# Performance work log

Measured on AMD Instinct MI355X. Metric: run time of the kernel, lower is better.

## Reference

```python
import jax, jax.numpy as jnp
import numpy as np

N, E, B, L, D, H = 50000, 800000, 64, 32, 256, 256


def setup_inputs() -> dict:
    key = jax.random.key(0)
    ks = jax.random.split(key, 20)
    s = 0.05
    inp = {
        'x': jax.random.normal(ks[0], (N, D), jnp.float32),
        'edge_index': jax.random.randint(ks[1], (2, E), 0, N),
        'batch': jnp.sort(jax.random.randint(ks[2], (N,), 0, B)),
        'paths': jax.random.randint(ks[3], (B, L), 0, N),
        # SAGEConv1: lin_l (aggregated neighbors, with bias) + lin_r (root, no bias)
        'w1l': jax.random.normal(ks[4], (D, H), jnp.float32) * s,
        'b1l': jnp.zeros((H,), jnp.float32),
        'w1r': jax.random.normal(ks[5], (D, H), jnp.float32) * s,
        # SAGEConv2
        'w2l': jax.random.normal(ks[6], (H, H), jnp.float32) * s,
        'b2l': jnp.zeros((H,), jnp.float32),
        'w2r': jax.random.normal(ks[7], (H, H), jnp.float32) * s,
        # LSTM (gate order i,f,g,o as in torch)
        'w_ih': jax.random.normal(ks[8], (4 * H, H), jnp.float32) * s,
        'w_hh': jax.random.normal(ks[9], (4 * H, H), jnp.float32) * s,
        'b_ih': jnp.zeros((4 * H,), jnp.float32),
        'b_hh': jnp.zeros((4 * H,), jnp.float32),
        # scorer MLP
        'wm1': jax.random.normal(ks[10], (2 * H, H), jnp.float32) * s,
        'bm1': jnp.zeros((H,), jnp.float32),
        'wm2': jax.random.normal(ks[11], (H, 1), jnp.float32) * s,
        'bm2': jnp.zeros((1,), jnp.float32),
    }
    return inp


def sage_conv(x, src, dst, wl, bl, wr):
    # mean-aggregate neighbor features (messages flow src -> dst)
    agg = jax.ops.segment_sum(x[src], dst, num_segments=N)
    deg = jax.ops.segment_sum(jnp.ones((src.shape[0],), x.dtype), dst, num_segments=N)
    mean = agg / jnp.maximum(deg, 1.0)[:, None]
    return mean @ wl + bl + x @ wr


def lstm_last_hidden(seq, w_ih, w_hh, b_ih, b_hh):
    # seq: [B, L, H] -> hn: [B, H]
    h0 = jnp.zeros((seq.shape[0], H), seq.dtype)
    c0 = jnp.zeros_like(h0)

    def step(carry, xt):
        h, c = carry
        gates = xt @ w_ih.T + b_ih + h @ w_hh.T + b_hh
        i, f, g, o = jnp.split(gates, 4, axis=-1)
        c = jax.nn.sigmoid(f) * c + jax.nn.sigmoid(i) * jnp.tanh(g)
        h = jax.nn.sigmoid(o) * jnp.tanh(c)
        return (h, c), None

    (hn, _), _ = jax.lax.scan(step, (h0, c0), jnp.swapaxes(seq, 0, 1))
    return hn


def reference(x, edge_index, batch, paths, w1l, b1l, w1r, w2l, b2l, w2r,
              w_ih, w_hh, b_ih, b_hh, wm1, bm1, wm2, bm2):
    src, dst = edge_index[0], edge_index[1]
    h = jax.nn.relu(sage_conv(x, src, dst, w1l, b1l, w1r))
    node_emb = sage_conv(h, src, dst, w2l, b2l, w2r)  # [N, H]

    # global mean pool per graph
    gsum = jax.ops.segment_sum(node_emb, batch, num_segments=B)
    gcnt = jax.ops.segment_sum(jnp.ones((N,), node_emb.dtype), batch, num_segments=B)
    graph_emb = gsum / jnp.maximum(gcnt, 1.0)[:, None]  # [B, H]

    path_seq = node_emb[paths]  # [B, L, H]
    path_emb = lstm_last_hidden(path_seq, w_ih, w_hh, b_ih, b_hh)  # [B, H]

    combined = jnp.concatenate([graph_emb, path_emb], axis=-1)  # [B, 2H]
    scores = jax.nn.relu(combined @ wm1 + bm1) @ wm2 + bm2  # [B, 1]
    return scores.reshape(-1)  # torch.cat of per-path [1] scores -> [B]
```

## Files before the change

kernel.cpp:

```cpp
#include <hip/hip_runtime.h>

namespace {

constexpr int NN = 50000;
constexpr int NE = 800000;
constexpr int NB = 64;
constexpr int NL = 32;
constexpr int ND = 256;
constexpr int NSCAN = 196;

typedef __attribute__((ext_vector_type(8))) short short8v;
typedef __attribute__((ext_vector_type(4))) float float4v;

__device__ __forceinline__ float sigf(float x){ return 1.0f/(1.0f + __expf(-x)); }

__device__ __forceinline__ ushort rne_bf16(float f){
  uint u = __float_as_uint(f);
  return (ushort)((u + 0x7FFFu + ((u >> 16) & 1u)) >> 16);
}
__device__ __forceinline__ float bf2f(ushort u){ return __uint_as_float((uint)u << 16); }

__device__ __forceinline__ void split8(float4 fa, float4 fb, uint4& h, uint4& lo){
  uint a0=__float_as_uint(fa.x), a1=__float_as_uint(fa.y), a2=__float_as_uint(fa.z), a3=__float_as_uint(fa.w);
  uint b0=__float_as_uint(fb.x), b1=__float_as_uint(fb.y), b2=__float_as_uint(fb.z), b3=__float_as_uint(fb.w);
  h.x = (a0>>16) | (a1 & 0xFFFF0000u);
  h.y = (a2>>16) | (a3 & 0xFFFF0000u);
  h.z = (b0>>16) | (b1 & 0xFFFF0000u);
  h.w = (b2>>16) | (b3 & 0xFFFF0000u);
  float r0 = fa.x - __uint_as_float(a0 & 0xFFFF0000u);
  float r1 = fa.y - __uint_as_float(a1 & 0xFFFF0000u);
  float r2 = fa.z - __uint_as_float(a2 & 0xFFFF0000u);
  float r3 = fa.w - __uint_as_float(a3 & 0xFFFF0000u);
  float r4 = fb.x - __uint_as_float(b0 & 0xFFFF0000u);
  float r5 = fb.y - __uint_as_float(b1 & 0xFFFF0000u);
  float r6 = fb.z - __uint_as_float(b2 & 0xFFFF0000u);
  float r7 = fb.w - __uint_as_float(b3 & 0xFFFF0000u);
  lo.x = (__float_as_uint(r0)>>16) | (__float_as_uint(r1) & 0xFFFF0000u);
  lo.y = (__float_as_uint(r2)>>16) | (__float_as_uint(r3) & 0xFFFF0000u);
  lo.z = (__float_as_uint(r4)>>16) | (__float_as_uint(r5) & 0xFFFF0000u);
  lo.w = (__float_as_uint(r6)>>16) | (__float_as_uint(r7) & 0xFFFF0000u);
}

__global__ void k_hist(const int* __restrict__ dst, int* __restrict__ cnt){
  int stride = gridDim.x * blockDim.x;
  for (int e = blockIdx.x*blockDim.x + threadIdx.x; e < NE; e += stride)
    atomicAdd(&cnt[dst[e]], 1);
}

__global__ void k_scan_block(const int* __restrict__ cnt, int* __restrict__ offs,
                             int* __restrict__ bsum){
  __shared__ int s[256];
  const int t = threadIdx.x, i = blockIdx.x*256 + t;
  int v = cnt[i];
  s[t] = v; __syncthreads();
  #pragma unroll
  for (int off = 1; off < 256; off <<= 1){
    int x = (t >= off) ? s[t-off] : 0;
    __syncthreads();
    s[t] += x;
    __syncthreads();
  }
  offs[i] = s[t] - v;
  if (t == 255) bsum[blockIdx.x] = s[255];
}

__global__ void k_scan_top(const int* __restrict__ bsum, int* __restrict__ bsum2){
  __shared__ int s[256];
  const int t = threadIdx.x;
  int v = (t < NSCAN) ? bsum[t] : 0;
  s[t] = v; __syncthreads();
  #pragma unroll
  for (int off = 1; off < 256; off <<= 1){
    int x = (t >= off) ? s[t-off] : 0;
    __syncthreads();
    s[t] += x;
    __syncthreads();
  }
  if (t < NSCAN) bsum2[t] = s[t] - v;
}

__global__ void k_scan_add(int* __restrict__ offs, const int* __restrict__ bsum2,
                           int* __restrict__ cursor){
  const int i = blockIdx.x*256 + threadIdx.x;
  int v = offs[i] + bsum2[blockIdx.x];
  offs[i] = v;
  cursor[i] = v;
}

__global__ void k_fill(const int* __restrict__ src, const int* __restrict__ dst,
                       int* __restrict__ cursor, int* __restrict__ csr){
  int stride = gridDim.x * blockDim.x;
  for (int e = blockIdx.x*blockDim.x + threadIdx.x; e < NE; e += stride){
    int d = dst[e];
    int pos = atomicAdd(&cursor[d], 1);
    csr[pos] = src[e];
  }
}

__global__ void k_tobf16(const float* __restrict__ in, ushort* __restrict__ out){
  const int i = blockIdx.x*blockDim.x + threadIdx.x;
  const float4 a = ((const float4*)in)[i*2];
  const float4 b = ((const float4*)in)[i*2+1];
  ushort o[8] = { rne_bf16(a.x), rne_bf16(a.y), rne_bf16(a.z), rne_bf16(a.w),
                  rne_bf16(b.x), rne_bf16(b.y), rne_bf16(b.z), rne_bf16(b.w) };
  ((uint4*)out)[i] = *(uint4*)o;
}

__launch_bounds__(256, 8)
__global__ void k_gather_bf16(const ushort* __restrict__ feat, const int* __restrict__ offs,
                              const int* __restrict__ csr, float* __restrict__ out){
  __shared__ float4 sp[256];
  const int u = blockIdx.x, t = threadIdx.x;
  const int w = t >> 6, l = t & 63;
  const int beg = offs[u], end = offs[u+1];
  const int lc = l * 4;
  float a0 = 0.f, a1 = 0.f, a2 = 0.f, a3 = 0.f;
  int e = beg + w;
  for (; e + 4 < end; e += 8){
    int s0 = csr[e], s1 = csr[e+4];
    ushort4 v0 = *(const ushort4*)(feat + (long long)s0*ND + lc);
    ushort4 v1 = *(const ushort4*)(feat + (long long)s1*ND + lc);
    a0 += bf2f(v0.x) + bf2f(v1.x);
    a1 += bf2f(v0.y) + bf2f(v1.y);
    a2 += bf2f(v0.z) + bf2f(v1.z);
    a3 += bf2f(v0.w) + bf2f(v1.w);
  }
  if (e < end){
    int s0 = csr[e];
    ushort4 v0 = *(const ushort4*)(feat + (long long)s0*ND + lc);
    a0 += bf2f(v0.x); a1 += bf2f(v0.y); a2 += bf2f(v0.z); a3 += bf2f(v0.w);
  }
  sp[t] = make_float4(a0, a1, a2, a3);
  __syncthreads();
  if (t < 64){
    float4 p0 = sp[t], p1 = sp[64+t], p2 = sp[128+t], p3 = sp[192+t];
    float inv = 1.0f / fmaxf((float)(end - beg), 1.0f);
    float4 r;
    r.x = (p0.x + p1.x + p2.x + p3.x) * inv;
    r.y = (p0.y + p1.y + p2.y + p3.y) * inv;
    r.z = (p0.z + p1.z + p2.z + p3.z) * inv;
    r.w = (p0.w + p1.w + p2.w + p3.w) * inv;
    *(float4*)(out + (long long)u*ND + t*4) = r;
  }
}

__global__ void k_wsplit(const float* __restrict__ wl, const float* __restrict__ wr,
                         ushort* __restrict__ WtH, ushort* __restrict__ WtL){
  const int k = blockIdx.x;
  const int n = threadIdx.x;
  float v = (k < 256) ? wl[k*256 + n] : wr[(k-256)*256 + n];
  uint u = __float_as_uint(v);
  float r = v - __uint_as_float(u & 0xFFFF0000u);
  const int wc = n >> 6, nt = (n >> 4) & 3, lm = n & 15;
  const int kk = k >> 5, lq = (k >> 3) & 3, j = k & 7;
  const long long idx = (long long)(((wc*4 + nt)*16 + kk)*64 + lq*16 + lm)*8 + j;
  WtH[idx] = (ushort)(u >> 16);
  WtL[idx] = (ushort)(__float_as_uint(r) >> 16);
}

__launch_bounds__(256, 2)
__global__ void k_gemm_mfma(const float* __restrict__ A1, const float* __restrict__ A2,
                            const ushort* __restrict__ WtH, const ushort* __restrict__ WtL,
                            const float* __restrict__ bias, float* __restrict__ C,
                            ushort* __restrict__ Cb, int relu)
{
  __shared__ float eb[16*260];
  const int t  = threadIdx.x;
  const int w  = t >> 6;
  const int l  = t & 63;
  const int lm = l & 15;
  const int lq = l >> 4;
  const int m0 = blockIdx.x * 64;

  const uint4* BH4 = (const uint4*)WtH;
  const uint4* BL4 = (const uint4*)WtL;

  const float4v vzero = {0.f, 0.f, 0.f, 0.f};
  float4v acc[4][4];
  #pragma unroll
  for (int i = 0; i < 4; ++i)
    #pragma unroll
    for (int j = 0; j < 4; ++j) acc[i][j] = vzero;

  long long arow[4];
  #pragma unroll
  for (int mt = 0; mt < 4; ++mt){
    int row = m0 + mt*16 + lm;
    row = (row < NN) ? row : (NN - 1);
    arow[mt] = (long long)row * ND;
  }
  int bbase[4];
  #pragma unroll
  for (int nt = 0; nt < 4; ++nt) bbase[nt] = (w*4 + nt)*1024 + l;

  auto ldB = [&](int kk, uint4* bh, uint4* bl){
    #pragma unroll
    for (int nt = 0; nt < 4; ++nt){
      int idx = bbase[nt] + kk*64;
      bh[nt] = BH4[idx];
      bl[nt] = BL4[idx];
    }
  };
  auto ldA = [&](int kk, uint4* ah, uint4* al){
    const float* Ab = (kk < 8) ? A1 : A2;
    const int koff = (kk & 7)*32 + lq*8;
    #pragma unroll
    for (int mt = 0; mt < 4; ++mt){
      const float* p = Ab + arow[mt] + koff;
      float4 fa = *(const float4*)p;
      float4 fb = *(const float4*)(p + 4);
      split8(fa, fb, ah[mt], al[mt]);
    }
  };

  uint4 bhb[2][4], blb[2][4], ahb[2][4], alb[2][4];
  ldB(0, bhb[0], blb[0]);
  ldA(0, ahb[0], alb[0]);

  #pragma unroll
  for (int kk = 0; kk < 16; ++kk){
    const int cur = kk & 1, nx = cur ^ 1;
    if (kk < 15){
      ldB(kk + 1, bhb[nx], blb[nx]);
      ldA(kk + 1, ahb[nx], alb[nx]);
    }
    #pragma unroll
    for (int nt = 0; nt < 4; ++nt){
      short8v bh = *(short8v*)&bhb[cur][nt];
      short8v bl = *(short8v*)&blb[cur][nt];
      #pragma unroll
      for (int mt = 0; mt < 4; ++mt){
        short8v ah = *(short8v*)&ahb[cur][mt];
        short8v al = *(short8v*)&alb[cur][mt];
        acc[mt][nt] = __builtin_amdgcn_mfma_f32_16x16x32_bf16(ah, bh, acc[mt][nt], 0, 0, 0);
        acc[mt][nt] = __builtin_amdgcn_mfma_f32_16x16x32_bf16(al, bh, acc[mt][nt], 0, 0, 0);
        acc[mt][nt] = __builtin_amdgcn_mfma_f32_16x16x32_bf16(ah, bl, acc[mt][nt], 0, 0, 0);
      }
    }
  }

  float bvv[4];
  #pragma unroll
  for (int nt = 0; nt < 4; ++nt) bvv[nt] = bias[w*64 + nt*16 + lm];

  #pragma unroll
  for (int mt = 0; mt < 4; ++mt){
    #pragma unroll
    for (int nt = 0; nt < 4; ++nt){
      #pragma unroll
      for (int r = 0; r < 4; ++r){
        float v = acc[mt][nt][r] + bvv[nt];
        if (relu) v = fmaxf(v, 0.f);
        eb[(lq*4 + r)*260 + w*64 + nt*16 + lm] = v;
      }
    }
    __syncthreads();
    #pragma unroll
    for (int i = 0; i < 4; ++i){
      int idx = i*256 + t;
      int rr  = idx >> 6;
      int c4  = (idx & 63) * 4;
      int grow = m0 + mt*16 + rr;
      if (grow < NN){
        float4 fv = *(float4*)&eb[rr*260 + c4];
        *(float4*)(C + (long long)grow*ND + c4) = fv;
        if (Cb){
          ushort ub[4] = { rne_bf16(fv.x), rne_bf16(fv.y), rne_bf16(fv.z), rne_bf16(fv.w) };
          *(ushort4*)(Cb + (long long)grow*ND + c4) = *(ushort4*)ub;
        }
      }
    }
    __syncthreads();
  }
}

__launch_bounds__(256, 3)
__global__ void k_xgate(const float* __restrict__ emb, const int* __restrict__ paths,
                        const float* __restrict__ w_ih, const float* __restrict__ b_ih,
                        const float* __restrict__ b_hh, float* __restrict__ xg)
{
  __shared__ float As[16][68];
  __shared__ float Ws[16][260];
  const int t  = threadIdx.x;
  const int m0 = blockIdx.x * 64;
  const int g0 = blockIdx.y * 256;
  const int rg = t >> 5, cg = t & 31;
  const int sm = t >> 2, sj = (t & 3) * 4;

  float acc[8][8];
  #pragma unroll
  for (int i = 0; i < 8; ++i)
    #pragma unroll
    for (int j = 0; j < 8; ++j) acc[i][j] = 0.f;

  const int node = paths[m0 + sm];
  const float* arow = emb  + (long long)node*ND;
  const float* wrow = w_ih + (long long)(g0 + t)*ND;

  for (int k0 = 0; k0 < 256; k0 += 16){
    float4 av = *(const float4*)(arow + k0 + sj);
    float4 q0 = *(const float4*)(wrow + k0 + 0);
    float4 q1 = *(const float4*)(wrow + k0 + 4);
    float4 q2 = *(const float4*)(wrow + k0 + 8);
    float4 q3 = *(const float4*)(wrow + k0 + 12);
    __syncthreads();
    As[sj+0][sm]=av.x; As[sj+1][sm]=av.y; As[sj+2][sm]=av.z; As[sj+3][sm]=av.w;
    Ws[ 0][t]=q0.x; Ws[ 1][t]=q0.y; Ws[ 2][t]=q0.z; Ws[ 3][t]=q0.w;
    Ws[ 4][t]=q1.x; Ws[ 5][t]=q1.y; Ws[ 6][t]=q1.z; Ws[ 7][t]=q1.w;
    Ws[ 8][t]=q2.x; Ws[ 9][t]=q2.y; Ws[10][t]=q2.z; Ws[11][t]=q2.w;
    Ws[12][t]=q3.x; Ws[13][t]=q3.y; Ws[14][t]=q3.z; Ws[15][t]=q3.w;
    __syncthreads();
    #pragma unroll
    for (int k = 0; k < 16; ++k){
      float a[8], b[8];
      *(float4*)&a[0] = *(const float4*)&As[k][rg*8];
      *(float4*)&a[4] = *(const float4*)&As[k][rg*8+4];
      *(float4*)&b[0] = *(const float4*)&Ws[k][cg*8];
      *(float4*)&b[4] = *(const float4*)&Ws[k][cg*8+4];
      #pragma unroll
      for (int i = 0; i < 8; ++i)
        #pragma unroll
        for (int j = 0; j < 8; ++j)
          acc[i][j] = fmaf(a[i], b[j], acc[i][j]);
    }
  }

  float bv[8];
  #pragma unroll
  for (int j = 0; j < 8; ++j){ int g = g0 + cg*8 + j; bv[j] = b_ih[g] + b_hh[g]; }
  #pragma unroll
  for (int i = 0; i < 8; ++i){
    int row = m0 + rg*8 + i;
    float o[8];
    #pragma unroll
    for (int j = 0; j < 8; ++j) o[j] = acc[i][j] + bv[j];
    *(float4*)(xg + (long long)row*1024 + g0 + cg*8 + 0) = *(float4*)&o[0];
    *(float4*)(xg + (long long)row*1024 + g0 + cg*8 + 4) = *(float4*)&o[4];
  }
}

__launch_bounds__(256, 4)
__global__ void k_lstm_step(const float* __restrict__ h_in, float* __restrict__ h_out,
                            float* __restrict__ c_state, const float* __restrict__ xg,
                            const float* __restrict__ w_hh, int tstep)
{
  __shared__ float ws[4*256];
  __shared__ float hs[32*260];
  __shared__ float part[2*128];
  __shared__ float gs[128];
  const int t  = threadIdx.x;
  const int u  = blockIdx.x >> 1;
  const int b0 = (blockIdx.x & 1) * 32;

  {
    int gate = t >> 6, c4 = (t & 63) * 4;
    float4 v = *(const float4*)(w_hh + (long long)(gate*256 + u)*256 + c4);
    *(float4*)&ws[gate*256 + c4] = v;
  }
  #pragma unroll
  for (int i = 0; i < 8; ++i){
    int idx = i*256 + t;
    int b = idx >> 6, c4 = (idx & 63) * 4;
    float4 v = *(const float4*)(h_in + (long long)(b0 + b)*256 + c4);
    *(float4*)&hs[b*260 + c4] = v;
  }
  __syncthreads();

  const int b  = t & 31;
  const int g  = (t >> 5) & 3;
  const int kd = t >> 7;
  float s = 0.f;
  const float* hp = &hs[b*260 + kd*128];
  const float* wp = &ws[g*256 + kd*128];
  #pragma unroll
  for (int k4 = 0; k4 < 32; ++k4){
    float4 h4 = *(const float4*)(hp + k4*4);
    float4 w4 = *(const float4*)(wp + k4*4);
    s += h4.x*w4.x + h4.y*w4.y + h4.z*w4.z + h4.w*w4.w;
  }
  part[kd*128 + b*4 + g] = s;
  __syncthreads();

  if (t < 128){
    int bb = t >> 2, gg = t & 3;
    const float* xp = xg + ((long long)(b0 + bb)*NL + tstep)*1024;
    gs[t] = part[t] + part[128 + t] + xp[gg*256 + u];
  }
  __syncthreads();

  if (t < 32){
    float gi = gs[t*4+0], gf = gs[t*4+1], gG = gs[t*4+2], go = gs[t*4+3];
    int bb = b0 + t;
    float c_old = c_state[bb*256 + u];
    float c_new = sigf(gf)*c_old + sigf(gi)*tanhf(gG);
    c_state[bb*256 + u] = c_new;
    h_out[bb*256 + u] = sigf(go)*tanhf(c_new);
  }
}

__global__ void k_pool(const float* __restrict__ emb, const int* __restrict__ batch,
                       float* __restrict__ gsum, float* __restrict__ gcnt)
{
  __shared__ int bs[256];
  const int t  = threadIdx.x;
  const int n0 = blockIdx.x * 256;
  {
    int n = n0 + t;
    bs[t] = (n < NN) ? batch[n] : -1;
  }
  __syncthreads();
  int cur = bs[0];
  float acc = 0.f; int cnt = 0;
  for (int j = 0; j < 256; ++j){
    int nn = n0 + j;
    if (nn >= NN) break;
    int g = bs[j];
    if (g != cur){
      unsafeAtomicAdd(&gsum[cur*256 + t], acc);
      if (t == 0) unsafeAtomicAdd(&gcnt[cur], (float)cnt);
      acc = 0.f; cnt = 0; cur = g;
    }
    acc += emb[(long long)nn*256 + t];
    ++cnt;
  }
  if (cnt > 0 && cur >= 0){
    unsafeAtomicAdd(&gsum[cur*256 + t], acc);
    if (t == 0) unsafeAtomicAdd(&gcnt[cur], (float)cnt);
  }
}

__global__ void k_score(const float* __restrict__ gsum, const float* __restrict__ gcnt,
                        const float* __restrict__ hfin, const float* __restrict__ wm1,
                        const float* __restrict__ bm1, const float* __restrict__ wm2,
                        const float* __restrict__ bm2, float* __restrict__ out)
{
  __shared__ float cs[512];
  __shared__ float red[4];
  const int b = blockIdx.x, t = threadIdx.x;
  float inv = 1.0f / fmaxf(gcnt[b], 1.0f);
  cs[t]       = gsum[b*256 + t] * inv;
  cs[256 + t] = hfin[b*256 + t];
  __syncthreads();
  float v = 0.f;
  #pragma unroll 4
  for (int k = 0; k < 512; ++k) v = fmaf(cs[k], wm1[(long long)k*256 + t], v);
  v = fmaxf(v + bm1[t], 0.f) * wm2[t];
  #pragma unroll
  for (int off = 32; off > 0; off >>= 1) v += __shfl_down(v, off, 64);
  if ((t & 63) == 0) red[t >> 6] = v;
  __syncthreads();
  if (t == 0) out[b] = red[0] + red[1] + red[2] + red[3] + bm2[0];
}

}

extern "C" void kernel_launch(void* const* d_in, const int* in_sizes, int n_in,
                              void* d_out, int out_size, void* d_ws, size_t ws_size,
                              hipStream_t stream)
{
  const float* x     = (const float*)d_in[0];
  const int*   eidx  = (const int*)  d_in[1];
  const int*   batch = (const int*)  d_in[2];
  const int*   paths = (const int*)  d_in[3];
  const float* w1l   = (const float*)d_in[4];
  const float* b1l   = (const float*)d_in[5];
  const float* w1r   = (const float*)d_in[6];
  const float* w2l   = (const float*)d_in[7];
  const float* b2l   = (const float*)d_in[8];
  const float* w2r   = (const float*)d_in[9];
  const float* w_ih  = (const float*)d_in[10];
  const float* w_hh  = (const float*)d_in[11];
  const float* b_ih  = (const float*)d_in[12];
  const float* b_hh  = (const float*)d_in[13];
  const float* wm1   = (const float*)d_in[14];
  const float* bm1   = (const float*)d_in[15];
  const float* wm2   = (const float*)d_in[16];
  const float* bm2   = (const float*)d_in[17];

  const int* src = eidx;
  const int* dst = eidx + NE;

  float* w    = (float*)d_ws;
  float* bufA = w;
  float* bufB = bufA + (long long)NN*ND;
  float* xg   = bufB + (long long)NN*ND;
  float* gsum = xg   + 2048*1024;
  float* gcnt = gsum + NB*ND;
  float* h0   = gcnt + 64;
  float* c0   = h0   + NB*ND;
  float* h1   = c0   + NB*ND;
  ushort* wt1H = (ushort*)(h1 + NB*ND);
  ushort* wt1L = wt1H + 256*512;
  ushort* wt2H = wt1L + 256*512;
  ushort* wt2L = wt2H + 256*512;
  ushort* fb16 = wt2L + 256*512;

  int* cnt    = (int*)xg;
  int* offs   = cnt    + 50432;
  int* cursor = offs   + 50432;
  int* bsum   = cursor + 50432;
  int* bsum2  = bsum   + 256;
  int* csr    = bsum2  + 256;

  k_wsplit<<<512, 256, 0, stream>>>(w1l, w1r, wt1H, wt1L);
  k_wsplit<<<512, 256, 0, stream>>>(w2l, w2r, wt2H, wt2L);

  k_tobf16<<<(NN*ND/8 + 255)/256, 256, 0, stream>>>(x, fb16);

  hipMemsetAsync(cnt, 0, 50432*sizeof(int), stream);
  k_hist<<<1024, 256, 0, stream>>>(dst, cnt);
  k_scan_block<<<NSCAN, 256, 0, stream>>>(cnt, offs, bsum);
  k_scan_top<<<1, 256, 0, stream>>>(bsum, bsum2);
  k_scan_add<<<NSCAN, 256, 0, stream>>>(offs, bsum2, cursor);
  k_fill<<<1024, 256, 0, stream>>>(src, dst, cursor, csr);

  k_gather_bf16<<<NN, 256, 0, stream>>>(fb16, offs, csr, bufA);
  k_gemm_mfma<<<(NN+63)/64, 256, 0, stream>>>(bufA, x, wt1H, wt1L, b1l, bufB, fb16, 1);

  k_gather_bf16<<<NN, 256, 0, stream>>>(fb16, offs, csr, bufA);
  k_gemm_mfma<<<(NN+63)/64, 256, 0, stream>>>(bufA, bufB, wt2H, wt2L, b2l, bufA, (ushort*)nullptr, 0);

  hipMemsetAsync(gsum, 0, (NB*ND + 64)*sizeof(float), stream);
  k_pool<<<(NN+255)/256, 256, 0, stream>>>(bufA, batch, gsum, gcnt);

  k_xgate<<<dim3((NB*NL)/64, 1024/256), 256, 0, stream>>>(bufA, paths, w_ih, b_ih, b_hh, xg);

  hipMemsetAsync(h0, 0, 2*(size_t)NB*ND*sizeof(float), stream);
  for (int ts = 0; ts < NL; ++ts){
    float* hin  = (ts & 1) ? h1 : h0;
    float* hout = (ts & 1) ? h0 : h1;
    k_lstm_step<<<512, 256, 0, stream>>>(hin, hout, c0, xg, w_hh, ts);
  }

  k_score<<<NB, 256, 0, stream>>>(gsum, gcnt, h0, wm1, bm1, wm2, bm2, (float*)d_out);
}
```

Before: 852.3 us.

## Store activations as pre-split bf16 hi/lo and stage GEMM A-tiles via LDS

```diff
diff --git a/kernel.cpp b/kernel.cpp
--- a/kernel.cpp
+++ b/kernel.cpp
@@ -12,6 +12,10 @@
 typedef __attribute__((ext_vector_type(8))) short short8v;
 typedef __attribute__((ext_vector_type(4))) float float4v;
 
+#define GLD16(GP, LP) __builtin_amdgcn_global_load_lds( \
+    (const __attribute__((address_space(1))) void*)(GP), \
+    (__attribute__((address_space(3))) void*)(LP), 16, 0, 0)
+
 __device__ __forceinline__ float sigf(float x){ return 1.0f/(1.0f + __expf(-x)); }
 
 __device__ __forceinline__ ushort rne_bf16(float f){
@@ -19,6 +23,13 @@
   return (ushort)((u + 0x7FFFu + ((u >> 16) & 1u)) >> 16);
 }
 __device__ __forceinline__ float bf2f(ushort u){ return __uint_as_float((uint)u << 16); }
+
+__device__ __forceinline__ void split1(float f, ushort& h, ushort& lo){
+  uint u = __float_as_uint(f);
+  h = (ushort)(u >> 16);
+  float r = f - __uint_as_float(u & 0xFFFF0000u);
+  lo = (ushort)(__float_as_uint(r) >> 16);
+}
 
 __device__ __forceinline__ void split8(float4 fa, float4 fb, uint4& h, uint4& lo){
   uint a0=__float_as_uint(fa.x), a1=__float_as_uint(fa.y), a2=__float_as_uint(fa.z), a3=__float_as_uint(fa.w);
@@ -108,7 +119,8 @@
 
 __launch_bounds__(256, 8)
 __global__ void k_gather_bf16(const ushort* __restrict__ feat, const int* __restrict__ offs,
-                              const int* __restrict__ csr, float* __restrict__ out){
+                              const int* __restrict__ csr,
+                              ushort* __restrict__ outH, ushort* __restrict__ outL){
   __shared__ float4 sp[256];
   const int u = blockIdx.x, t = threadIdx.x;
   const int w = t >> 6, l = t & 63;
@@ -140,7 +152,13 @@
     r.y = (p0.y + p1.y + p2.y + p3.y) * inv;
     r.z = (p0.z + p1.z + p2.z + p3.z) * inv;
     r.w = (p0.w + p1.w + p2.w + p3.w) * inv;
-    *(float4*)(out + (long long)u*ND + t*4) = r;
+    ushort hh[4], ll[4];
+    split1(r.x, hh[0], ll[0]);
+    split1(r.y, hh[1], ll[1]);
+    split1(r.z, hh[2], ll[2]);
+    split1(r.w, hh[3], ll[3]);
+    *(ushort4*)(outH + (long long)u*ND + t*4) = *(ushort4*)hh;
+    *(ushort4*)(outL + (long long)u*ND + t*4) = *(ushort4*)ll;
   }
 }
 
@@ -158,13 +176,18 @@
   WtL[idx] = (ushort)(__float_as_uint(r) >> 16);
 }
 
-__launch_bounds__(256, 2)
-__global__ void k_gemm_mfma(const float* __restrict__ A1, const float* __restrict__ A2,
+__launch_bounds__(256, 3)
+__global__ void k_gemm_mfma(const ushort* __restrict__ A1H, const ushort* __restrict__ A1L,
+                            const ushort* __restrict__ A2H, const ushort* __restrict__ A2L,
+                            const float* __restrict__ A2F,
                             const ushort* __restrict__ WtH, const ushort* __restrict__ WtL,
-                            const float* __restrict__ bias, float* __restrict__ C,
-                            ushort* __restrict__ Cb, int relu)
+                            const float* __restrict__ bias,
+                            ushort* __restrict__ CH, ushort* __restrict__ CL,
+                            ushort* __restrict__ Cb, int relu, int a2f32)
 {
   __shared__ float eb[16*260];
+  char* const sm = (char*)eb;
+
   const int t  = threadIdx.x;
   const int w  = t >> 6;
   const int l  = t & 63;
@@ -182,61 +205,93 @@
     #pragma unroll
     for (int j = 0; j < 4; ++j) acc[i][j] = vzero;
 
-  long long arow[4];
-  #pragma unroll
-  for (int mt = 0; mt < 4; ++mt){
-    int row = m0 + mt*16 + lm;
-    row = (row < NN) ? row : (NN - 1);
-    arow[mt] = (long long)row * ND;
-  }
   int bbase[4];
   #pragma unroll
   for (int nt = 0; nt < 4; ++nt) bbase[nt] = (w*4 + nt)*1024 + l;
 
-  auto ldB = [&](int kk, uint4* bh, uint4* bl){
+  const int j0 = w * 2;
+
+  auto stageHL = [&](int bb, const ushort* __restrict__ H, const ushort* __restrict__ L, int k0){
+    #pragma unroll
+    for (int jj = 0; jj < 2; ++jj){
+      const int j   = j0 + jj;
+      const int arr = j >> 2;
+      const int i   = j & 3;
+      const int row = i*16 + (l >> 2);
+      int rg = m0 + row; rg = (rg < NN) ? rg : (NN - 1);
+      const int g = (l & 3) ^ ((row >> 1) & 3);
+      const ushort* srcp = (arr ? L : H) + (long long)rg*ND + k0 + g*8;
+      GLD16(srcp, sm + bb + arr*4096 + i*1024);
+    }
+  };
+  auto stageF = [&](int bb, int k0){
+    #pragma unroll
+    for (int jj = 0; jj < 2; ++jj){
+      const int j   = j0 + jj;
+      const int row = j*8 + (l >> 3);
+      int rg = m0 + row; rg = (rg < NN) ? rg : (NN - 1);
+      const int g = (l & 7) ^ (row & 7);
+      const float* srcp = A2F + (long long)rg*ND + k0 + g*4;
+      GLD16(srcp, sm + bb + j*1024);
+    }
+  };
+  auto stage = [&](int bb, int kk){
+    if (kk < 8)      stageHL(bb, A1H, A1L, kk*32);
+    else if (!a2f32) stageHL(bb, A2H, A2L, (kk - 8)*32);
+    else             stageF (bb, (kk - 8)*32);
+  };
+
+  stage(0, 0);
+  __syncthreads();
+
+  #pragma unroll
+  for (int kk = 0; kk < 16; ++kk){
+    const int bb = (kk & 1) * 8192;
+
+    uint4 bh[4], bl[4];
     #pragma unroll
     for (int nt = 0; nt < 4; ++nt){
-      int idx = bbase[nt] + kk*64;
+      const int idx = bbase[nt] + kk*64;
       bh[nt] = BH4[idx];
       bl[nt] = BL4[idx];
     }
-  };
-  auto ldA = [&](int kk, uint4* ah, uint4* al){
-    const float* Ab = (kk < 8) ? A1 : A2;
-    const int koff = (kk & 7)*32 + lq*8;
-    #pragma unroll
-    for (int mt = 0; mt < 4; ++mt){
-      const float* p = Ab + arow[mt] + koff;
-      float4 fa = *(const float4*)p;
-      float4 fb = *(const float4*)(p + 4);
-      split8(fa, fb, ah[mt], al[mt]);
-    }
-  };
-
-  uint4 bhb[2][4], blb[2][4], ahb[2][4], alb[2][4];
-  ldB(0, bhb[0], blb[0]);
-  ldA(0, ahb[0], alb[0]);
-
-  #pragma unroll
-  for (int kk = 0; kk < 16; ++kk){
-    const int cur = kk & 1, nx = cur ^ 1;
-    if (kk < 15){
-      ldB(kk + 1, bhb[nx], blb[nx]);
-      ldA(kk + 1, ahb[nx], alb[nx]);
-    }
-    #pragma unroll
-    for (int nt = 0; nt < 4; ++nt){
-      short8v bh = *(short8v*)&bhb[cur][nt];
-      short8v bl = *(short8v*)&blb[cur][nt];
+
+    if (kk < 15) stage(bb ^ 8192, kk + 1);
+
+    uint4 ah[4], al[4];
+    if (kk < 8 || !a2f32){
       #pragma unroll
       for (int mt = 0; mt < 4; ++mt){
-        short8v ah = *(short8v*)&ahb[cur][mt];
-        short8v al = *(short8v*)&alb[cur][mt];
-        acc[mt][nt] = __builtin_amdgcn_mfma_f32_16x16x32_bf16(ah, bh, acc[mt][nt], 0, 0, 0);
-        acc[mt][nt] = __builtin_amdgcn_mfma_f32_16x16x32_bf16(al, bh, acc[mt][nt], 0, 0, 0);
-        acc[mt][nt] = __builtin_amdgcn_mfma_f32_16x16x32_bf16(ah, bl, acc[mt][nt], 0, 0, 0);
+        const int row = mt*16 + lm;
+        const int off = bb + row*64 + ((lq ^ ((row >> 1) & 3)) << 4);
+        ah[mt] = *(const uint4*)(sm + off);
+        al[mt] = *(const uint4*)(sm + 4096 + off);
       }
-    }
+    } else {
+      #pragma unroll
+      for (int mt = 0; mt < 4; ++mt){
+        const int row = mt*16 + lm;
+        const int s = row & 7;
+        const float4 fa = *(const float4*)(sm + bb + row*128 + (((2*lq    ) ^ s) << 4));
+        const float4 fb = *(const float4*)(sm + bb + row*128 + (((2*lq + 1) ^ s) << 4));
+        split8(fa, fb, ah[mt], al[mt]);
+      }
+    }
+
+    #pragma unroll
+    for (int nt = 0; nt < 4; ++nt){
+      short8v bhv = *(short8v*)&bh[nt];
+      short8v blv = *(short8v*)&bl[nt];
+      #pragma unroll
+      for (int mt = 0; mt < 4; ++mt){
+        short8v ahv = *(short8v*)&ah[mt];
+        short8v alv = *(short8v*)&al[mt];
+        acc[mt][nt] = __builtin_amdgcn_mfma_f32_16x16x32_bf16(ahv, bhv, acc[mt][nt], 0, 0, 0);
+        acc[mt][nt] = __builtin_amdgcn_mfma_f32_16x16x32_bf16(alv, bhv, acc[mt][nt], 0, 0, 0);
+        acc[mt][nt] = __builtin_amdgcn_mfma_f32_16x16x32_bf16(ahv, blv, acc[mt][nt], 0, 0, 0);
+      }
+    }
+    __syncthreads();
   }
 
   float bvv[4];
@@ -263,7 +318,13 @@
       int grow = m0 + mt*16 + rr;
       if (grow < NN){
         float4 fv = *(float4*)&eb[rr*260 + c4];
-        *(float4*)(C + (long long)grow*ND + c4) = fv;
+        ushort hh[4], ll[4];
+        split1(fv.x, hh[0], ll[0]);
+        split1(fv.y, hh[1], ll[1]);
+        split1(fv.z, hh[2], ll[2]);
+        split1(fv.w, hh[3], ll[3]);
+        *(ushort4*)(CH + (long long)grow*ND + c4) = *(ushort4*)hh;
+        *(ushort4*)(CL + (long long)grow*ND + c4) = *(ushort4*)ll;
         if (Cb){
           ushort ub[4] = { rne_bf16(fv.x), rne_bf16(fv.y), rne_bf16(fv.z), rne_bf16(fv.w) };
           *(ushort4*)(Cb + (long long)grow*ND + c4) = *(ushort4*)ub;
@@ -275,7 +336,8 @@
 }
 
 __launch_bounds__(256, 3)
-__global__ void k_xgate(const float* __restrict__ emb, const int* __restrict__ paths,
+__global__ void k_xgate(const ushort* __restrict__ EH, const ushort* __restrict__ EL,
+                        const int* __restrict__ paths,
                         const float* __restrict__ w_ih, const float* __restrict__ b_ih,
                         const float* __restrict__ b_hh, float* __restrict__ xg)
 {
@@ -294,17 +356,23 @@
     for (int j = 0; j < 8; ++j) acc[i][j] = 0.f;
 
   const int node = paths[m0 + sm];
-  const float* arow = emb  + (long long)node*ND;
+  const ushort* ehrow = EH + (long long)node*ND;
+  const ushort* elrow = EL + (long long)node*ND;
   const float* wrow = w_ih + (long long)(g0 + t)*ND;
 
   for (int k0 = 0; k0 < 256; k0 += 16){
-    float4 av = *(const float4*)(arow + k0 + sj);
+    ushort4 hv = *(const ushort4*)(ehrow + k0 + sj);
+    ushort4 lv = *(const ushort4*)(elrow + k0 + sj);
+    float av0 = bf2f(hv.x) + bf2f(lv.x);
+    float av1 = bf2f(hv.y) + bf2f(lv.y);
+    float av2 = bf2f(hv.z) + bf2f(lv.z);
+    float av3 = bf2f(hv.w) + bf2f(lv.w);
     float4 q0 = *(const float4*)(wrow + k0 + 0);
     float4 q1 = *(const float4*)(wrow + k0 + 4);
     float4 q2 = *(const float4*)(wrow + k0 + 8);
     float4 q3 = *(const float4*)(wrow + k0 + 12);
     __syncthreads();
-    As[sj+0][sm]=av.x; As[sj+1][sm]=av.y; As[sj+2][sm]=av.z; As[sj+3][sm]=av.w;
+    As[sj+0][sm]=av0; As[sj+1][sm]=av1; As[sj+2][sm]=av2; As[sj+3][sm]=av3;
     Ws[ 0][t]=q0.x; Ws[ 1][t]=q0.y; Ws[ 2][t]=q0.z; Ws[ 3][t]=q0.w;
     Ws[ 4][t]=q1.x; Ws[ 5][t]=q1.y; Ws[ 6][t]=q1.z; Ws[ 7][t]=q1.w;
     Ws[ 8][t]=q2.x; Ws[ 9][t]=q2.y; Ws[10][t]=q2.z; Ws[11][t]=q2.w;
@@ -398,7 +466,8 @@
   }
 }
 
-__global__ void k_pool(const float* __restrict__ emb, const int* __restrict__ batch,
+__global__ void k_pool(const ushort* __restrict__ EH, const ushort* __restrict__ EL,
+                       const int* __restrict__ batch,
                        float* __restrict__ gsum, float* __restrict__ gcnt)
 {
   __shared__ int bs[256];
@@ -420,7 +489,7 @@
       if (t == 0) unsafeAtomicAdd(&gcnt[cur], (float)cnt);
       acc = 0.f; cnt = 0; cur = g;
     }
-    acc += emb[(long long)nn*256 + t];
+    acc += bf2f(EH[(long long)nn*256 + t]) + bf2f(EL[(long long)nn*256 + t]);
     ++cnt;
   }
   if (cnt > 0 && cur >= 0){
@@ -495,6 +564,11 @@
   ushort* wt2L = wt2H + 256*512;
   ushort* fb16 = wt2L + 256*512;
 
+  ushort* A1H = (ushort*)bufA;
+  ushort* A1L = A1H + (long long)NN*ND;
+  ushort* h1H = (ushort*)bufB;
+  ushort* h1L = h1H + (long long)NN*ND;
+
   int* cnt    = (int*)xg;
   int* offs   = cnt    + 50432;
   int* cursor = offs   + 50432;
@@ -514,16 +588,18 @@
   k_scan_add<<<NSCAN, 256, 0, stream>>>(offs, bsum2, cursor);
   k_fill<<<1024, 256, 0, stream>>>(src, dst, cursor, csr);
 
-  k_gather_bf16<<<NN, 256, 0, stream>>>(fb16, offs, csr, bufA);
-  k_gemm_mfma<<<(NN+63)/64, 256, 0, stream>>>(bufA, x, wt1H, wt1L, b1l, bufB, fb16, 1);
-
-  k_gather_bf16<<<NN, 256, 0, stream>>>(fb16, offs, csr, bufA);
-  k_gemm_mfma<<<(NN+63)/64, 256, 0, stream>>>(bufA, bufB, wt2H, wt2L, b2l, bufA, (ushort*)nullptr, 0);
+  k_gather_bf16<<<NN, 256, 0, stream>>>(fb16, offs, csr, A1H, A1L);
+  k_gemm_mfma<<<(NN+63)/64, 256, 0, stream>>>(A1H, A1L, nullptr, nullptr, x,
+                                              wt1H, wt1L, b1l, h1H, h1L, fb16, 1, 1);
+
+  k_gather_bf16<<<NN, 256, 0, stream>>>(fb16, offs, csr, A1H, A1L);
+  k_gemm_mfma<<<(NN+63)/64, 256, 0, stream>>>(A1H, A1L, h1H, h1L, nullptr,
+                                              wt2H, wt2L, b2l, h1H, h1L, (ushort*)nullptr, 0, 0);
 
   hipMemsetAsync(gsum, 0, (NB*ND + 64)*sizeof(float), stream);
-  k_pool<<<(NN+255)/256, 256, 0, stream>>>(bufA, batch, gsum, gcnt);
-
-  k_xgate<<<dim3((NB*NL)/64, 1024/256), 256, 0, stream>>>(bufA, paths, w_ih, b_ih, b_hh, xg);
+  k_pool<<<(NN+255)/256, 256, 0, stream>>>(h1H, h1L, batch, gsum, gcnt);
+
+  k_xgate<<<dim3((NB*NL)/64, 1024/256), 256, 0, stream>>>(h1H, h1L, paths, w_ih, b_ih, b_hh, xg);
 
   hipMemsetAsync(h0, 0, 2*(size_t)NB*ND*sizeof(float), stream);
   for (int ts = 0; ts < NL; ++ts){
```

Result: no change. 849.2 us (-0.4%).
